# Kernel tuning notes

Measured on AMD Instinct MI355X. Metric: run time of the kernel, lower is better.

Reference implementation:

```python
import jax, jax.numpy as jnp
import numpy as np

DIMENSIONS = 1000
NUM_LEVELS = 10
SIZE = 28
BATCH = 256
NUM_CLASSES = 10


def setup_inputs() -> dict:
    key = jax.random.key(0)
    k1, k2, k3 = jax.random.split(key, 3)
    # pixel values in [0, 1]
    x = jax.random.uniform(k1, (BATCH, SIZE, SIZE), dtype=jnp.float32)
    # fixed bipolar position hypervectors (bundle of x/y Level HVs); use +-1 like MAP HVs
    position = jnp.where(jax.random.normal(k2, (SIZE * SIZE, DIMENSIONS)) > 0, 1.0, -1.0).astype(jnp.float32)
    # Level value embedding table
    value_table = jnp.where(jax.random.normal(k3, (NUM_LEVELS, DIMENSIONS)) > 0, 1.0, -1.0).astype(jnp.float32)
    # classifier weight, initialized to zero in the original module
    W = jnp.zeros((NUM_CLASSES, DIMENSIONS), dtype=jnp.float32)
    return {"x": x, "position": position, "value_table": value_table, "W": W}


def reference(x, position, value_table, W):
    B = x.shape[0]
    xf = x.reshape(B, -1)  # [B, P] flatten
    # torchhd Level value_to_index with low=0, high=1
    idx = jnp.clip(jnp.round(xf * (NUM_LEVELS - 1)), 0, NUM_LEVELS - 1).astype(jnp.int32)
    hv = value_table[idx]                         # gather: [B, P, D]
    bound = position[None, :, :] * hv             # bind:   [B, P, D]
    s = jnp.sum(bound, axis=1)                    # multiset sum over pixels: [B, D]
    enc = jnp.where(s > 0, 1.0, -1.0).astype(x.dtype)  # hard_quantize
    logit = enc @ W.T                             # [B, num_classes]
    return logit
```

## Files before the change

### kernel.cpp

```cpp
#include <hip/hip_runtime.h>
#include <stdint.h>

#define DIMS   1000
#define NLEV   10
#define NPIX   784
#define NBATCH 256
#define NCLS   10
#define WPD    32

__global__ __launch_bounds__(256) void pack_ballot(const float* __restrict__ position,
                                                   const float* __restrict__ value_table,
                                                   uint64_t* __restrict__ ws64) {
    const int t    = threadIdx.x;
    const int lane = t & 63;
    const int wv   = (blockIdx.x * 256 + t) >> 6;
    const int nw   = (gridDim.x * 256) >> 6;
    for (int r = wv; r < NPIX + NLEV; r += nw) {
        const float* src = (r < NPIX) ? (position + (size_t)r * DIMS)
                                      : (value_table + (size_t)(r - NPIX) * DIMS);
        #pragma unroll
        for (int k = 0; k < 16; ++k) {
            int d = k * 64 + lane;
            float v = (d < DIMS) ? src[d] : 0.f;
            uint64_t m = __ballot(v > 0.f);
            if (lane == 0) ws64[(size_t)r * 16 + k] = m;
        }
    }
}

__device__ __forceinline__ void fa(uint32_t a, uint32_t b, uint32_t cin,
                                   uint32_t& s, uint32_t& c) {
    uint32_t t = a ^ b;
    s = t ^ cin;
    c = (a & b) | (t & cin);
}

__global__ __launch_bounds__(512) void hdc_main(const float* __restrict__ x,
                                                const float* __restrict__ W,
                                                const uint32_t* __restrict__ ws_bits,
                                                float* __restrict__ out) {
    __shared__ uint32_t s_idx[NPIX];
    __shared__ uint32_t s_vt[NLEV * WPD];
    __shared__ uint32_t s_cnt1[32 * 8 * 7];
    __shared__ uint32_t s_cnt2[32 * 4 * 8];
    __shared__ uint32_t s_cnt3[32 * 2 * 9];
    __shared__ uint32_t s_cnt4_enc[32];
    __shared__ float    s_red[8][NCLS];

    const int b = blockIdx.x;
    const int t = threadIdx.x;

    for (int p = t; p < NPIX; p += 512) {
        float v = x[b * NPIX + p] * 9.0f;
        int l = (int)rintf(v);
        l = l < 0 ? 0 : (l > 9 ? 9 : l);
        s_idx[p] = (uint32_t)(l * WPD);
    }
    if (t < NLEV * WPD) s_vt[t] = ws_bits[NPIX * WPD + t];
    __syncthreads();

    const int w = t & 31;
    const int g = t >> 5;

    uint32_t p0 = 0, p1 = 0, p2 = 0, p3 = 0, p4 = 0, p5 = 0;

    for (int c = 0; c < 6; ++c) {
        uint32_t idxv[8], posv[8], xv[8];
        #pragma unroll
        for (int j = 0; j < 8; ++j)
            idxv[j] = s_idx[g + 128 * c + 16 * j];
        #pragma unroll
        for (int j = 0; j < 8; ++j)
            posv[j] = ws_bits[(g + 128 * c + 16 * j) * WPD + w];
        #pragma unroll
        for (int j = 0; j < 8; ++j)
            xv[j] = posv[j] ^ s_vt[idxv[j] + w];
        uint32_t sa, ca, sb, cb, sc, cc, sd, cd, se, ce, sf, cf, cg;
        fa(xv[0], xv[1], xv[2], sa, ca);
        fa(xv[3], xv[4], xv[5], sb, cb);
        fa(xv[6], xv[7], p0,   sc, cc);
        fa(sa, sb, sc, p0, cd);
        fa(ca, cb, cc, se, ce);
        fa(se, cd, p1, p1, cf);
        fa(ce, cf, p2, p2, cg);
        uint32_t tmp = p3 & cg; p3 ^= cg;
        uint32_t tm2 = p4 & tmp; p4 ^= tmp;
        p5 ^= tm2;
    }
    {
        uint32_t xb = ws_bits[(g + 768) * WPD + w] ^ s_vt[s_idx[g + 768] + w];
        uint32_t c = xb, tmp;
        tmp = p0 & c; p0 ^= c; c = tmp;
        tmp = p1 & c; p1 ^= c; c = tmp;
        tmp = p2 & c; p2 ^= c; c = tmp;
        tmp = p3 & c; p3 ^= c; c = tmp;
        tmp = p4 & c; p4 ^= c; c = tmp;
        p5 ^= c;
    }

    {
        uint32_t q0 = __shfl_down(p0, 32), q1 = __shfl_down(p1, 32),
                 q2 = __shfl_down(p2, 32), q3 = __shfl_down(p3, 32),
                 q4 = __shfl_down(p4, 32), q5 = __shfl_down(p5, 32);
        uint32_t r0, r1, r2, r3, r4, r5, r6, c, tt;
        c  = p0 & q0; r0 = p0 ^ q0;
        tt = p1 ^ q1; r1 = tt ^ c; c = (p1 & q1) | (tt & c);
        tt = p2 ^ q2; r2 = tt ^ c; c = (p2 & q2) | (tt & c);
        tt = p3 ^ q3; r3 = tt ^ c; c = (p3 & q3) | (tt & c);
        tt = p4 ^ q4; r4 = tt ^ c; c = (p4 & q4) | (tt & c);
        tt = p5 ^ q5; r5 = tt ^ c; c = (p5 & q5) | (tt & c);
        r6 = c;
        const int wid = t >> 6;
        if ((t & 63) < 32) {
            int base = (w * 8 + wid) * 7;
            s_cnt1[base + 0] = r0; s_cnt1[base + 1] = r1; s_cnt1[base + 2] = r2;
            s_cnt1[base + 3] = r3; s_cnt1[base + 4] = r4; s_cnt1[base + 5] = r5;
            s_cnt1[base + 6] = r6;
        }
    }
    __syncthreads();

    if (t < 128) {
        int w2 = t & 31, j = t >> 5;
        int ba = (w2 * 8 + 2 * j) * 7, bb = (w2 * 8 + 2 * j + 1) * 7;
        uint32_t c = 0, tt;
        int bo = (w2 * 4 + j) * 8;
        #pragma unroll
        for (int i = 0; i < 7; ++i) {
            uint32_t a = s_cnt1[ba + i], bv = s_cnt1[bb + i];
            tt = a ^ bv; s_cnt2[bo + i] = tt ^ c; c = (a & bv) | (tt & c);
        }
        s_cnt2[bo + 7] = c;
    }
    __syncthreads();

    if (t < 64) {
        int w2 = t & 31, j = t >> 5;
        int ba = (w2 * 4 + 2 * j) * 8, bb = (w2 * 4 + 2 * j + 1) * 8;
        uint32_t c = 0, tt;
        int bo = (w2 * 2 + j) * 9;
        #pragma unroll
        for (int i = 0; i < 8; ++i) {
            uint32_t a = s_cnt2[ba + i], bv = s_cnt2[bb + i];
            tt = a ^ bv; s_cnt3[bo + i] = tt ^ c; c = (a & bv) | (tt & c);
        }
        s_cnt3[bo + 8] = c;
    }
    __syncthreads();

    if (t < 32) {
        int ba = (t * 2) * 9, bb = (t * 2 + 1) * 9;
        uint32_t cnt[10];
        uint32_t c = 0, tt;
        #pragma unroll
        for (int i = 0; i < 9; ++i) {
            uint32_t a = s_cnt3[ba + i], bv = s_cnt3[bb + i];
            tt = a ^ bv; cnt[i] = tt ^ c; c = (a & bv) | (tt & c);
        }
        cnt[9] = c;
        uint32_t cy = 0;
        cy = cnt[3];
        cy = cnt[4] | cy;
        cy = cnt[5] | cy;
        cy = cnt[6] | cy;
        cy = cnt[7] & cy;
        cy = cnt[8] & cy;
        cy = cnt[9] | cy;
        s_cnt4_enc[t] = ~cy;
    }
    __syncthreads();

    float partial[NCLS];
    #pragma unroll
    for (int cc = 0; cc < NCLS; ++cc) partial[cc] = 0.f;

    if (t < 500) {
        int d0 = 2 * t;
        uint32_t ew = s_cnt4_enc[d0 >> 5];
        float e0 = ((ew >> (d0 & 31)) & 1u) ? 1.0f : -1.0f;
        float e1 = ((ew >> ((d0 + 1) & 31)) & 1u) ? 1.0f : -1.0f;
        #pragma unroll
        for (int cc = 0; cc < NCLS; ++cc) {
            const float2* wv = (const float2*)(W + cc * DIMS + d0);
            float2 wl = *wv;
            partial[cc] = e0 * wl.x + e1 * wl.y;
        }
    }
    #pragma unroll
    for (int cc = 0; cc < NCLS; ++cc) {
        #pragma unroll
        for (int off = 32; off > 0; off >>= 1)
            partial[cc] += __shfl_down(partial[cc], off);
    }
    const int lane = t & 63, wid = t >> 6;
    if (lane == 0) {
        #pragma unroll
        for (int cc = 0; cc < NCLS; ++cc) s_red[wid][cc] = partial[cc];
    }
    __syncthreads();
    if (t < NCLS) {
        float acc = 0.f;
        #pragma unroll
        for (int v = 0; v < 8; ++v) acc += s_red[v][t];
        out[b * NCLS + t] = acc;
    }
}

extern "C" void kernel_launch(void* const* d_in, const int* in_sizes, int n_in,
                              void* d_out, int out_size, void* d_ws, size_t ws_size,
                              hipStream_t stream) {
    const float* x        = (const float*)d_in[0];
    const float* position = (const float*)d_in[1];
    const float* vtab     = (const float*)d_in[2];
    const float* W        = (const float*)d_in[3];
    float* out            = (float*)d_out;

    pack_ballot<<<200, 256, 0, stream>>>(position, vtab, (uint64_t*)d_ws);
    hdc_main<<<NBATCH, 512, 0, stream>>>(x, W, (const uint32_t*)d_ws, out);
}
```

Baseline: 72.24 us.

## Fuse bit-packing into main kernel with a grid-wide atomic barrier

Removes the separate pack_ballot launch and folds its work into the main kernel. Each block packs up to eight position rows into global workspace, and packs the value table directly into shared memory. A global atomic counter acts as a grid-wide barrier before any block reads the packed position bits. This drops one kernel launch and the global round-trip for the value table. The barrier relies on all 256 blocks being co-resident, and its flag reset assumes the workspace starts at zero, at a 0xAA poison pattern, or at the count left by the previous call.

```diff
diff --git a/kernel.cpp b/kernel.cpp
--- a/kernel.cpp
+++ b/kernel.cpp
@@ -7,26 +7,7 @@
 #define NBATCH 256
 #define NCLS   10
 #define WPD    32
-
-__global__ __launch_bounds__(256) void pack_ballot(const float* __restrict__ position,
-                                                   const float* __restrict__ value_table,
-                                                   uint64_t* __restrict__ ws64) {
-    const int t    = threadIdx.x;
-    const int lane = t & 63;
-    const int wv   = (blockIdx.x * 256 + t) >> 6;
-    const int nw   = (gridDim.x * 256) >> 6;
-    for (int r = wv; r < NPIX + NLEV; r += nw) {
-        const float* src = (r < NPIX) ? (position + (size_t)r * DIMS)
-                                      : (value_table + (size_t)(r - NPIX) * DIMS);
-        #pragma unroll
-        for (int k = 0; k < 16; ++k) {
-            int d = k * 64 + lane;
-            float v = (d < DIMS) ? src[d] : 0.f;
-            uint64_t m = __ballot(v > 0.f);
-            if (lane == 0) ws64[(size_t)r * 16 + k] = m;
-        }
-    }
-}
+#define FLAG_IDX 65536
 
 __device__ __forceinline__ void fa(uint32_t a, uint32_t b, uint32_t cin,
                                    uint32_t& s, uint32_t& c) {
@@ -35,33 +16,76 @@
     c = (a & b) | (t & cin);
 }
 
-__global__ __launch_bounds__(512) void hdc_main(const float* __restrict__ x,
-                                                const float* __restrict__ W,
-                                                const uint32_t* __restrict__ ws_bits,
-                                                float* __restrict__ out) {
+__global__ __launch_bounds__(512) void hdc_fused(
+        const float* __restrict__ x, const float* __restrict__ position,
+        const float* __restrict__ vtab, const float* __restrict__ W,
+        uint32_t* __restrict__ ws, float* __restrict__ out) {
     __shared__ uint32_t s_idx[NPIX];
     __shared__ uint32_t s_vt[NLEV * WPD];
     __shared__ uint32_t s_cnt1[32 * 8 * 7];
     __shared__ uint32_t s_cnt2[32 * 4 * 8];
     __shared__ uint32_t s_cnt3[32 * 2 * 9];
-    __shared__ uint32_t s_cnt4_enc[32];
+    __shared__ uint32_t s_enc[32];
     __shared__ float    s_red[8][NCLS];
 
-    const int b = blockIdx.x;
-    const int t = threadIdx.x;
-
+    const int b    = blockIdx.x;
+    const int t    = threadIdx.x;
+    const int lane = t & 63;
+    const int wv   = t >> 6;
+
+    {
+        int row = b + 256 * wv;
+        if (row < NPIX) {
+            const float* src = position + (size_t)row * DIMS;
+            uint64_t* ws64 = (uint64_t*)ws;
+            #pragma unroll
+            for (int k = 0; k < 16; ++k) {
+                int d = k * 64 + lane;
+                float v = (d < DIMS) ? src[d] : 0.f;
+                uint64_t m = __ballot(v > 0.f);
+                if (lane == 0) ws64[(size_t)row * 16 + k] = m;
+            }
+        }
+    }
+    #pragma unroll
+    for (int e = 0; e < 2; ++e) {
+        int lev = 2 * wv + e;
+        if (lev < NLEV) {
+            const float* src = vtab + (size_t)lev * DIMS;
+            #pragma unroll
+            for (int k = 0; k < 16; ++k) {
+                int d = k * 64 + lane;
+                float v = (d < DIMS) ? src[d] : 0.f;
+                uint64_t m = __ballot(v > 0.f);
+                if (lane == 0) {
+                    s_vt[lev * WPD + 2 * k]     = (uint32_t)m;
+                    s_vt[lev * WPD + 2 * k + 1] = (uint32_t)(m >> 32);
+                }
+            }
+        }
+    }
     for (int p = t; p < NPIX; p += 512) {
         float v = x[b * NPIX + p] * 9.0f;
         int l = (int)rintf(v);
         l = l < 0 ? 0 : (l > 9 ? 9 : l);
         s_idx[p] = (uint32_t)(l * WPD);
     }
-    if (t < NLEV * WPD) s_vt[t] = ws_bits[NPIX * WPD + t];
-    __syncthreads();
+
+    __threadfence();
+    __syncthreads();
+    if (t == 0) {
+        uint32_t* flag = ws + FLAG_IDX;
+        atomicCAS(flag, 0xAAAAAAAAu, 0u);
+        atomicCAS(flag, (uint32_t)NBATCH, 0u);
+        atomicAdd(flag, 1u);
+        while (atomicAdd(flag, 0u) < (uint32_t)NBATCH)
+            __builtin_amdgcn_s_sleep(2);
+    }
+    __syncthreads();
+    __threadfence();
 
     const int w = t & 31;
     const int g = t >> 5;
-
     uint32_t p0 = 0, p1 = 0, p2 = 0, p3 = 0, p4 = 0, p5 = 0;
 
     for (int c = 0; c < 6; ++c) {
@@ -71,11 +95,11 @@
             idxv[j] = s_idx[g + 128 * c + 16 * j];
         #pragma unroll
         for (int j = 0; j < 8; ++j)
-            posv[j] = ws_bits[(g + 128 * c + 16 * j) * WPD + w];
+            posv[j] = ws[(g + 128 * c + 16 * j) * WPD + w];
         #pragma unroll
         for (int j = 0; j < 8; ++j)
             xv[j] = posv[j] ^ s_vt[idxv[j] + w];
-        uint32_t sa, ca, sb, cb, sc, cc, sd, cd, se, ce, sf, cf, cg;
+        uint32_t sa, ca, sb, cb, sc, cc, cd, se, ce, cf, cg;
         fa(xv[0], xv[1], xv[2], sa, ca);
         fa(xv[3], xv[4], xv[5], sb, cb);
         fa(xv[6], xv[7], p0,   sc, cc);
@@ -88,7 +112,7 @@
         p5 ^= tm2;
     }
     {
-        uint32_t xb = ws_bits[(g + 768) * WPD + w] ^ s_vt[s_idx[g + 768] + w];
+        uint32_t xb = ws[(g + 768) * WPD + w] ^ s_vt[s_idx[g + 768] + w];
         uint32_t c = xb, tmp;
         tmp = p0 & c; p0 ^= c; c = tmp;
         tmp = p1 & c; p1 ^= c; c = tmp;
@@ -158,7 +182,7 @@
             tt = a ^ bv; cnt[i] = tt ^ c; c = (a & bv) | (tt & c);
         }
         cnt[9] = c;
-        uint32_t cy = 0;
+        uint32_t cy;
         cy = cnt[3];
         cy = cnt[4] | cy;
         cy = cnt[5] | cy;
@@ -166,7 +190,7 @@
         cy = cnt[7] & cy;
         cy = cnt[8] & cy;
         cy = cnt[9] | cy;
-        s_cnt4_enc[t] = ~cy;
+        s_enc[t] = ~cy;
     }
     __syncthreads();
 
@@ -176,13 +200,13 @@
 
     if (t < 500) {
         int d0 = 2 * t;
-        uint32_t ew = s_cnt4_enc[d0 >> 5];
+        uint32_t ew = s_enc[d0 >> 5];
         float e0 = ((ew >> (d0 & 31)) & 1u) ? 1.0f : -1.0f;
         float e1 = ((ew >> ((d0 + 1) & 31)) & 1u) ? 1.0f : -1.0f;
         #pragma unroll
         for (int cc = 0; cc < NCLS; ++cc) {
-            const float2* wv = (const float2*)(W + cc * DIMS + d0);
-            float2 wl = *wv;
+            const float2* wvp = (const float2*)(W + cc * DIMS + d0);
+            float2 wl = *wvp;
             partial[cc] = e0 * wl.x + e1 * wl.y;
         }
     }
@@ -192,7 +216,7 @@
         for (int off = 32; off > 0; off >>= 1)
             partial[cc] += __shfl_down(partial[cc], off);
     }
-    const int lane = t & 63, wid = t >> 6;
+    const int wid = t >> 6;
     if (lane == 0) {
         #pragma unroll
         for (int cc = 0; cc < NCLS; ++cc) s_red[wid][cc] = partial[cc];
@@ -215,6 +239,6 @@
     const float* W        = (const float*)d_in[3];
     float* out            = (float*)d_out;
 
-    pack_ballot<<<200, 256, 0, stream>>>(position, vtab, (uint64_t*)d_ws);
-    hdc_main<<<NBATCH, 512, 0, stream>>>(x, W, (const uint32_t*)d_ws, out);
+    hdc_fused<<<NBATCH, 512, 0, stream>>>(x, position, vtab, W,
+                                          (uint32_t*)d_ws, out);
 }
```

Result: slower. 158.1 us (+118.9%).
